# Kernel tuning notes

Hardware: AMD Instinct MI355X
Metric: run time of the kernel (lower is better)

Reference implementation:

```python
import jax, jax.numpy as jnp
import numpy as np

FS = 44100
LS = 1323000  # 30 s at 44.1 kHz (Ls/fs = 30 exactly)
FMIN, FMAX, BNDS = 32.7, 20000.0, 96
MIN_WIN = 4


def _design():
    """Reimplementation of LogScale + nsgfwin(sliced=False) + calcwinrange +
    the matrixform nsgtf loop parameters, producing a dense gather-index
    matrix idx [nbins, Mmax] and window matrix gw [nbins, Mmax]."""
    odiv = (np.log2(FMAX) - np.log2(FMIN)) / (BNDS - 1)
    pow2n = 2.0 ** odiv
    f = FMIN * pow2n ** np.arange(BNDS)
    lbas = BNDS
    frqs = np.concatenate(([0.0], f, [FS / 2.0]))
    fbas = np.concatenate((frqs, FS - frqs[-2:0:-1]))  # mirror negative freqs
    fbas *= float(LS) / FS
    # bandwidths M (window lengths)
    M = np.zeros(len(fbas), dtype=np.int64)
    M[0] = np.round(2 * fbas[1])
    for k in range(1, 2 * lbas + 1):
        M[k] = np.round(fbas[k + 1] - fbas[k - 1])
    M[-1] = np.round(LS - fbas[-2])
    M = np.maximum(M, MIN_WIN)
    # Hann windows (zero-frequency centered, hannwin)
    g = [0.5 * (np.cos(np.arange(m) * (2.0 * np.pi / m)) + 1.0) for m in M]
    # center positions rfbas (calcwinrange -> timepos == rfbas, nn == Ls)
    fb = fbas.copy()
    fb[lbas] = (fbas[lbas - 1] + fbas[lbas + 1]) / 2
    fb[lbas + 2] = LS - fb[lbas]
    rfbas = np.round(fb).astype(np.int64)
    nbins = len(g) // 2 + 1        # real=True, reducedform=0
    Mmax = int(M[:nbins].max())    # matrixform: all bins padded to Mmax
    idx = np.zeros((nbins, Mmax), dtype=np.int32)
    gw = np.zeros((nbins, Mmax), dtype=np.float32)
    for j in range(nbins):
        gj = g[j]
        Lg = len(gj)
        win = (np.arange(-(Lg // 2), Lg - (Lg // 2)) + rfbas[j]) % LS
        gs = np.fft.fftshift(gj)  # g is real -> conj is a no-op
        h1, h2 = (Lg + 1) // 2, Lg // 2
        # nsgtf placement: temp[:h1] = t[h2:], temp[-h2:] = t[:h2]
        idx[j, :h1] = win[h2:]
        gw[j, :h1] = gs[h2:]
        if h2 > 0:
            idx[j, Mmax - h2:] = win[:h2]
            gw[j, Mmax - h2:] = gs[:h2]
    return idx, gw


def setup_inputs() -> dict:
    key = jax.random.key(0)
    idx, gw = _design()
    s = jax.random.normal(key, (2, LS), dtype=jnp.float32)  # [channels, Ls]
    return {"s": s, "idx": jnp.asarray(idx), "gw": jnp.asarray(gw)}


def reference(s, idx, gw):
    # NSGT forward (nsgtf, matrixform, real): FFT the signal, gather each
    # frequency bin's circular window range, multiply by the fftshifted
    # window, zero-pad into a length-Mmax buffer, and IFFT per bin.
    ft = jnp.fft.fft(s.astype(jnp.complex64))          # [B, Ls]
    t = ft[:, idx] * gw                                # [B, nbins, Mmax]
    c = jnp.fft.ifft(t, axis=-1)                       # complex coefficients
    # pack complex output as trailing (real, imag) float32 channel
    return jnp.stack((c.real, c.imag), axis=-1)        # [B, nbins, Mmax, 2]
```

## Files before the change

### kernel.cpp

```cpp
#include <hip/hip_runtime.h>

#define LS 1323000
#define NB 98
#define MM 123000
#define N2 3000
#define BATCH 2
#define NROWS_T (NB*BATCH)
#define TWO_PI 6.28318530717958647692f

#define KBN 188
#define QN  96
#define SROW (KBN*QN*16)
#define QP  104

typedef __attribute__((ext_vector_type(8))) short short8;
typedef __attribute__((ext_vector_type(4))) float f32x4;

__device__ __forceinline__ float2 cmul(float2 a, float2 b){
  return make_float2(a.x*b.x - a.y*b.y, a.x*b.y + a.y*b.x);
}
__device__ __forceinline__ unsigned short f2bf(float f){
  unsigned int u = __float_as_uint(f);
  unsigned int r = (u + 0x7FFFu + ((u >> 16) & 1u)) >> 16;
  return (unsigned short)r;
}

template<int R,int S>
__device__ __forceinline__ void butterfly(float2* v){
  if constexpr (R==2){
    float2 a=v[0], b=v[1];
    v[0]=make_float2(a.x+b.x, a.y+b.y);
    v[1]=make_float2(a.x-b.x, a.y-b.y);
  } else if constexpr (R==4){
    float2 t0=make_float2(v[0].x+v[2].x, v[0].y+v[2].y);
    float2 t1=make_float2(v[0].x-v[2].x, v[0].y-v[2].y);
    float2 t2=make_float2(v[1].x+v[3].x, v[1].y+v[3].y);
    float2 t3=make_float2(v[1].x-v[3].x, v[1].y-v[3].y);
    v[0]=make_float2(t0.x+t2.x, t0.y+t2.y);
    v[2]=make_float2(t0.x-t2.x, t0.y-t2.y);
    v[1]=make_float2(t1.x - (float)S*t3.y, t1.y + (float)S*t3.x);
    v[3]=make_float2(t1.x + (float)S*t3.y, t1.y - (float)S*t3.x);
  } else if constexpr (R==8){
    float2 e[4]={v[0],v[2],v[4],v[6]};
    float2 o[4]={v[1],v[3],v[5],v[7]};
    butterfly<4,S>(e);
    butterfly<4,S>(o);
    const float h = 0.70710678118654752440f;
    float2 w1=make_float2(h, (float)S*h);
    float2 w2=make_float2(0.f, (float)S);
    float2 w3=make_float2(-h, (float)S*h);
    float2 o1=cmul(o[1],w1), o2=cmul(o[2],w2), o3=cmul(o[3],w3);
    v[0]=make_float2(e[0].x+o[0].x, e[0].y+o[0].y);
    v[4]=make_float2(e[0].x-o[0].x, e[0].y-o[0].y);
    v[1]=make_float2(e[1].x+o1.x, e[1].y+o1.y);
    v[5]=make_float2(e[1].x-o1.x, e[1].y-o1.y);
    v[2]=make_float2(e[2].x+o2.x, e[2].y+o2.y);
    v[6]=make_float2(e[2].x-o2.x, e[2].y-o2.y);
    v[3]=make_float2(e[3].x+o3.x, e[3].y+o3.y);
    v[7]=make_float2(e[3].x-o3.x, e[7-4].y-o3.y);
    v[7]=make_float2(e[3].x-o3.x, e[3].y-o3.y);
  } else {
    float2 x[R];
    #pragma unroll
    for(int k=0;k<R;k++){
      float2 acc=v[0];
      #pragma unroll
      for(int n=1;n<R;n++){
        const int p=(k*n)%R;
        float ang = (float)S * (TWO_PI/(float)R) * (float)p;
        float sn,cs; __sincosf(ang,&sn,&cs);
        acc.x += v[n].x*cs - v[n].y*sn;
        acc.y += v[n].x*sn + v[n].y*cs;
      }
      x[k]=acc;
    }
    #pragma unroll
    for(int k=0;k<R;k++) v[k]=x[k];
  }
}

template<int R,int S>
__global__ void __launch_bounds__(256)
fft_pass(const float2* __restrict__ in, float2* __restrict__ out,
         int N, int Ns, int nrows){
  const int T = N / R;
  long long gid = (long long)blockIdx.x*blockDim.x + threadIdx.x;
  if (gid >= (long long)T*nrows) return;
  int row = (int)(gid / T);
  int j   = (int)(gid - (long long)row*T);
  const float2* x = in  + (size_t)row*N;
  float2*       y = out + (size_t)row*N;
  int t = j % Ns;
  float u = (float)t / (float)(Ns*R);
  float ang = (float)S * TWO_PI * u;
  float sn,cs; __sincosf(ang,&sn,&cs);
  float2 w1=make_float2(cs,sn);
  float2 wr=make_float2(1.f,0.f);
  float2 v[R];
  #pragma unroll
  for(int r=0;r<R;r++){
    float2 a = x[j + r*T];
    v[r] = cmul(a, wr);
    wr = cmul(wr, w1);
  }
  butterfly<R,S>(v);
  int d = (j/Ns)*(Ns*R) + t;
  #pragma unroll
  for(int r=0;r<R;r++) y[d + r*Ns] = v[r];
}

__global__ void __launch_bounds__(256)
fft_r2c8(const float* __restrict__ s, float2* __restrict__ y){
  const int T = LS/8;
  long long gid = (long long)blockIdx.x*blockDim.x + threadIdx.x;
  if (gid >= (long long)T*BATCH) return;
  int row = (int)(gid / T);
  int j   = (int)(gid - (long long)row*T);
  const float* x = s + (size_t)row*LS;
  float2*      yr = y + (size_t)row*LS;
  float2 v[8];
  #pragma unroll
  for(int r=0;r<8;r++) v[r] = make_float2(x[j + r*T], 0.f);
  butterfly<8,-1>(v);
  int d = 8*j;
  #pragma unroll
  for(int r=0;r<8;r++) yr[d + r] = v[r];
}

__global__ void span_init(int* __restrict__ spanA, int* __restrict__ spanB){
  int j = blockIdx.x*blockDim.x + threadIdx.x;
  if (j < NB){ spanA[j] = 0; spanB[j] = MM; }
}

#define SPAN_SLICE 4096
__global__ void __launch_bounds__(256)
rowspan_par(const float* __restrict__ gw, int* __restrict__ spanA,
            int* __restrict__ spanB){
  const int j  = blockIdx.x;
  const int lo = blockIdx.y * SPAN_SLICE;
  const int end = min(lo + SPAN_SLICE, MM);
  const float* g = gw + (size_t)j*MM;
  const int tid = threadIdx.x;
  int mA = -1, mB = MM;
  for (int m = lo + tid*4; m < end; m += 256*4){
    float4 v = *(const float4*)(g + m);
    #pragma unroll
    for (int t = 0; t < 4; t++){
      float f = ((const float*)&v)[t];
      int m2 = m + t;
      if (f != 0.f){
        if (m2 < 61500){ if (m2 > mA) mA = m2; }
        else           { if (m2 < mB) mB = m2; }
      }
    }
  }
  __shared__ int sA[256], sB[256];
  sA[tid]=mA; sB[tid]=mB; __syncthreads();
  for (int s=128; s>0; s>>=1){
    if (tid<s){ sA[tid]=max(sA[tid],sA[tid+s]); sB[tid]=min(sB[tid],sB[tid+s]); }
    __syncthreads();
  }
  if (tid==0){
    if (sA[0] >= 0) atomicMax(&spanA[j], sA[0]+1);
    if (sB[0] < MM) atomicMin(&spanB[j], sB[0]);
  }
}

__global__ void __launch_bounds__(256)
a_prep(unsigned short* __restrict__ A96){
  int i = blockIdx.x*blockDim.x + threadIdx.x;
  if (i >= 96*QP) return;
  int R = i / QP, q = i - R*QP;
  float val = 0.f;
  if (R < 82 && q < 82){
    int k2 = R >> 1, c = R & 1, n2 = q >> 1, cp = q & 1;
    int p = (k2*n2) % 41;
    float ang = (float)p * (TWO_PI/41.f);
    float sn, cs; __sincosf(ang, &sn, &cs);
    val = c ? (cp ? cs : sn) : (cp ? -sn : cs);
  }
  A96[i] = f2bf(val);
}

#define PTILE 1681
__global__ void __launch_bounds__(256)
pack_gather(const float2* __restrict__ ft, const int* __restrict__ idx,
            const float* __restrict__ gw, const int* __restrict__ spanA,
            const int* __restrict__ spanB, float2* __restrict__ T, int row0){
  const int row  = row0 + blockIdx.y;
  const int jrow = row % NB;
  const int b    = row / NB;
  const int spA = spanA[jrow], spB = spanB[jrow];
  const int base = blockIdx.x * PTILE;
  const int end  = min(base + PTILE, MM);
  if (!(base < spA || end > spB)) return;
  __shared__ float2 tile[PTILE];
  const int cnt = end - base;
  const int*   idxr = idx + (size_t)jrow*MM;
  const float* gwr  = gw  + (size_t)jrow*MM;
  const float2* ftb = ft  + (size_t)b*LS;
  for (int l = threadIdx.x; l < cnt; l += 256){
    int n = base + l;
    float g = gwr[n] * (1.0f/(float)MM);
    float2 f = ftb[idxr[n]];
    tile[l] = make_float2(f.x*g, f.y*g);
  }
  __syncthreads();
  float2* Trow = T + (size_t)blockIdx.y*MM;
  const int bm = base % 41;
  for (int l2 = threadIdx.x; l2 < PTILE; l2 += 256){
    int n2 = l2 / 41, w = l2 - 41*n2;
    int l0 = n2 - bm; if (l0 < 0) l0 += 41;
    int l = l0 + 41*w;
    if (l < cnt){
      int n = base + l;
      if (n < spA || n >= spB){
        int ig = n / 41;
        Trow[(size_t)n2*N2 + ig] = tile[l];
      }
    }
  }
}

template<int R, int Ns>
__device__ __forceinline__ void lds_stage(const float2* src, float2* dst, int tid){
  const int T = N2 / R;
  for (int j = tid; j < T; j += 256){
    int t = j % Ns;
    float2 w1;
    if constexpr (Ns == 1) w1 = make_float2(1.f, 0.f);
    else {
      float ang = TWO_PI * (float)t / (float)(Ns*R);
      float sn, cs; __sincosf(ang, &sn, &cs);
      w1 = make_float2(cs, sn);
    }
    float2 wr = make_float2(1.f, 0.f);
    float2 v[R];
    #pragma unroll
    for (int r = 0; r < R; r++){ v[r] = cmul(src[j + r*T], wr); wr = cmul(wr, w1); }
    butterfly<R,1>(v);
    int d = (j/Ns)*(Ns*R) + t;
    #pragma unroll
    for (int r = 0; r < R; r++) dst[d + r*Ns] = v[r];
  }
}

__global__ void __launch_bounds__(256)
inv_s1(const float2* __restrict__ T, const int* __restrict__ spanA,
       const int* __restrict__ spanB,
       unsigned short* __restrict__ Bb, int row0){
  __shared__ float2 u0[N2];
  __shared__ float2 u1[N2];
  const int n2  = blockIdx.x;
  const int row = row0 + blockIdx.y;
  const int jrow = row % NB;
  const int tid = threadIdx.x;
  const int spA = spanA[jrow], spB = spanB[jrow];
  const int n1A = (spA - n2 + 40) / 41;
  const int n1B = (spB - n2 + 40) / 41;
  const float2* Trow = T + (size_t)blockIdx.y*MM + (size_t)n2*N2;
  for (int i = tid; i < N2; i += 256){
    float2 val = make_float2(0.f, 0.f);
    if (i < n1A || i >= n1B) val = Trow[i];
    u0[i] = val;
  }
  __syncthreads();
  lds_stage<5,1>(u0, u1, tid);   __syncthreads();
  lds_stage<5,5>(u1, u0, tid);   __syncthreads();
  lds_stage<5,25>(u0, u1, tid);  __syncthreads();
  lds_stage<3,125>(u1, u0, tid); __syncthreads();
  lds_stage<8,375>(u0, u1, tid); __syncthreads();
  unsigned short* Brow = Bb + (size_t)blockIdx.y*SROW;
  const int qr = 2*n2, qi = 2*n2+1;
  for (int k1 = tid; k1 < N2; k1 += 256){
    float ang = (float)(n2*k1) * (TWO_PI/(float)MM);
    float sn, cs; __sincosf(ang, &sn, &cs);
    float2 v = cmul(u1[k1], make_float2(cs, sn));
    int kb = k1 >> 4, kl = k1 & 15;
    size_t base = (size_t)kb*(QN*16) + kl;
    Brow[base + qr*16] = f2bf(v.x);
    Brow[base + qi*16] = f2bf(v.y);
  }
}

__global__ void __launch_bounds__(256)
inv_s2_mfma(const unsigned short* __restrict__ A96,
            const unsigned short* __restrict__ Bb,
            float2* __restrict__ out){
  __shared__ unsigned short Als[96*QP];
  __shared__ unsigned short Bls[64*QP];
  const int tid = threadIdx.x;

  {
    const uint4* src = (const uint4*)A96;
    uint4* dst = (uint4*)Als;
    for (int f = tid; f < (96*QP*2)/16; f += 256) dst[f] = src[f];
  }
  {
    const unsigned short* Bt = Bb + (size_t)blockIdx.y*SROW
                                  + (size_t)blockIdx.x*4*(QN*16);
    for (int f = tid; f < 768; f += 256){
      uint4 d = *(const uint4*)(Bt + (size_t)f*8);
      int q   = (f >> 1) % QN;
      int kb  = f / (QN*2);
      int kl0 = (f & 1) * 8;
      if (q >= 82) d = make_uint4(0u,0u,0u,0u);
      const unsigned short* e = (const unsigned short*)&d;
      int rbase = kb*16 + kl0;
      #pragma unroll
      for (int j = 0; j < 8; j++)
        Bls[(rbase + j)*QP + q] = e[j];
    }
  }
  __syncthreads();

  const int w = tid >> 6, l = tid & 63;
  const int g = l >> 4, c = l & 15;

  f32x4 acc[6];
  #pragma unroll
  for (int m = 0; m < 6; m++) acc[m] = (f32x4){0.f,0.f,0.f,0.f};

  short8 b0 = *(const short8*)&Bls[(16*w + c)*QP +  0 + 8*g];
  short8 b1 = *(const short8*)&Bls[(16*w + c)*QP + 32 + 8*g];
  short8 b2 = *(const short8*)&Bls[(16*w + c)*QP + 64 + 8*g];
  #pragma unroll
  for (int m = 0; m < 6; m++){
    short8 a0 = *(const short8*)&Als[(16*m + c)*QP +  0 + 8*g];
    short8 a1 = *(const short8*)&Als[(16*m + c)*QP + 32 + 8*g];
    short8 a2 = *(const short8*)&Als[(16*m + c)*QP + 64 + 8*g];
    acc[m] = __builtin_amdgcn_mfma_f32_16x16x32_bf16(a0, b0, acc[m], 0, 0, 0);
    acc[m] = __builtin_amdgcn_mfma_f32_16x16x32_bf16(a1, b1, acc[m], 0, 0, 0);
    acc[m] = __builtin_amdgcn_mfma_f32_16x16x32_bf16(a2, b2, acc[m], 0, 0, 0);
  }

  float2* orow = out + (size_t)blockIdx.y*MM;
  int k1 = blockIdx.x*64 + 16*w + c;
  if (k1 < N2){
    #pragma unroll
    for (int m = 0; m < 6; m++){
      int R0 = 16*m + 4*g;
      int k2a = R0 >> 1;
      int k2b = k2a + 1;
      if (k2a < 41) orow[(size_t)k2a*N2 + k1] = make_float2(acc[m][0], acc[m][1]);
      if (k2b < 41) orow[(size_t)k2b*N2 + k1] = make_float2(acc[m][2], acc[m][3]);
    }
  }
}

extern "C" void kernel_launch(void* const* d_in, const int* in_sizes, int n_in,
                              void* d_out, int out_size, void* d_ws, size_t ws_size,
                              hipStream_t stream){
  const float* s   = (const float*)d_in[0];
  const int*   idx = (const int*)d_in[1];
  const float* gw  = (const float*)d_in[2];
  float2* out = (float2*)d_out;
  char* ws = (char*)d_ws;

  const size_t FWD_BYTES = 21168128;
  float2* bufA = (float2*)ws;
  float2* bufB = (float2*)(ws + FWD_BYTES);
  int* spanA = (int*)(ws + 2*FWD_BYTES);
  int* spanB = (int*)(ws + 2*FWD_BYTES + 512);
  unsigned short* A96 = (unsigned short*)(ws + 2*FWD_BYTES + 1024);
  const size_t A_BYTES = 20480;
  unsigned short* Bbase = (unsigned short*)(ws + 2*FWD_BYTES + 1024 + A_BYTES);

  a_prep<<<(96*QP + 255)/256, 256, 0, stream>>>(A96);
  span_init<<<1, 128, 0, stream>>>(spanA, spanB);
  {
    dim3 g(NB, (MM + SPAN_SLICE - 1)/SPAN_SLICE);
    rowspan_par<<<g, 256, 0, stream>>>(gw, spanA, spanB);
  }

  {
    long long tot = (long long)(LS/8)*BATCH;
    int blks = (int)((tot + 255)/256);
    fft_r2c8<<<blks,256,0,stream>>>(s, bufA);
  }
  float2* cur = bufA; float2* nxt = bufB;
  int Ns = 8;
  #define FWD(R) do{                                                         \
    long long tot = (long long)(LS/(R))*BATCH;                               \
    int blks = (int)((tot + 255)/256);                                       \
    fft_pass<R,-1><<<blks,256,0,stream>>>(cur, nxt, LS, Ns, BATCH);          \
    Ns *= (R);                                                               \
    { float2* tmp=cur; cur=nxt; nxt=tmp; }                                   \
  }while(0)
  FWD(7); FWD(7); FWD(5); FWD(5); FWD(5); FWD(3); FWD(3); FWD(3);
  #undef FWD

  const size_t row_bytes = (size_t)SROW * 2;
  size_t used = 2*FWD_BYTES + 1024 + A_BYTES;
  size_t avail = (ws_size > used) ? (ws_size - used) : 0;
  int max_chunk = (int)(avail / row_bytes);
  if (max_chunk > NROWS_T) max_chunk = NROWS_T;
  if (max_chunk < 1) max_chunk = 1;

  const int ptiles = (MM + PTILE - 1)/PTILE;
  for (int c0 = 0; c0 < NROWS_T; c0 += max_chunk){
    int cr = NROWS_T - c0; if (cr > max_chunk) cr = max_chunk;
    float2* Tchunk = out + (size_t)c0*MM;
    dim3 g0(ptiles, cr);
    pack_gather<<<g0,256,0,stream>>>(cur, idx, gw, spanA, spanB, Tchunk, c0);
    dim3 g1(41, cr);
    inv_s1<<<g1,256,0,stream>>>(Tchunk, spanA, spanB, Bbase, c0);
    dim3 g2(47, cr);
    inv_s2_mfma<<<g2,256,0,stream>>>(A96, Bbase, Tchunk);
  }
}
```

Measured before the change: 542.7 us.

## Pack both real channels into one complex FFT and precompute inverse twiddle tables

```diff
diff --git a/kernel.cpp b/kernel.cpp
--- a/kernel.cpp
+++ b/kernel.cpp
@@ -13,6 +13,12 @@
 #define SROW (KBN*QN*16)
 #define QP  104
 
+#define TBL2_OFF 0
+#define TBL3_OFF 20
+#define TBL4_OFF 120
+#define TBL5_OFF 370
+#define TBL_N    2995
+
 typedef __attribute__((ext_vector_type(8))) short short8;
 typedef __attribute__((ext_vector_type(4))) float f32x4;
 
@@ -27,11 +33,7 @@
 
 template<int R,int S>
 __device__ __forceinline__ void butterfly(float2* v){
-  if constexpr (R==2){
-    float2 a=v[0], b=v[1];
-    v[0]=make_float2(a.x+b.x, a.y+b.y);
-    v[1]=make_float2(a.x-b.x, a.y-b.y);
-  } else if constexpr (R==4){
+  if constexpr (R==4){
     float2 t0=make_float2(v[0].x+v[2].x, v[0].y+v[2].y);
     float2 t1=make_float2(v[0].x-v[2].x, v[0].y-v[2].y);
     float2 t2=make_float2(v[1].x+v[3].x, v[1].y+v[3].y);
@@ -57,7 +59,6 @@
     v[2]=make_float2(e[2].x+o2.x, e[2].y+o2.y);
     v[6]=make_float2(e[2].x-o2.x, e[2].y-o2.y);
     v[3]=make_float2(e[3].x+o3.x, e[3].y+o3.y);
-    v[7]=make_float2(e[3].x-o3.x, e[7-4].y-o3.y);
     v[7]=make_float2(e[3].x-o3.x, e[3].y-o3.y);
   } else {
     float2 x[R];
@@ -82,14 +83,10 @@
 template<int R,int S>
 __global__ void __launch_bounds__(256)
 fft_pass(const float2* __restrict__ in, float2* __restrict__ out,
-         int N, int Ns, int nrows){
+         int N, int Ns){
   const int T = N / R;
-  long long gid = (long long)blockIdx.x*blockDim.x + threadIdx.x;
-  if (gid >= (long long)T*nrows) return;
-  int row = (int)(gid / T);
-  int j   = (int)(gid - (long long)row*T);
-  const float2* x = in  + (size_t)row*N;
-  float2*       y = out + (size_t)row*N;
+  int j = blockIdx.x*blockDim.x + threadIdx.x;
+  if (j >= T) return;
   int t = j % Ns;
   float u = (float)t / (float)(Ns*R);
   float ang = (float)S * TWO_PI * u;
@@ -99,32 +96,30 @@
   float2 v[R];
   #pragma unroll
   for(int r=0;r<R;r++){
-    float2 a = x[j + r*T];
+    float2 a = in[j + r*T];
     v[r] = cmul(a, wr);
     wr = cmul(wr, w1);
   }
   butterfly<R,S>(v);
   int d = (j/Ns)*(Ns*R) + t;
   #pragma unroll
-  for(int r=0;r<R;r++) y[d + r*Ns] = v[r];
-}
-
-__global__ void __launch_bounds__(256)
-fft_r2c8(const float* __restrict__ s, float2* __restrict__ y){
+  for(int r=0;r<R;r++) out[d + r*Ns] = v[r];
+}
+
+__global__ void __launch_bounds__(256)
+fft_c2c8(const float* __restrict__ s, float2* __restrict__ y){
   const int T = LS/8;
-  long long gid = (long long)blockIdx.x*blockDim.x + threadIdx.x;
-  if (gid >= (long long)T*BATCH) return;
-  int row = (int)(gid / T);
-  int j   = (int)(gid - (long long)row*T);
-  const float* x = s + (size_t)row*LS;
-  float2*      yr = y + (size_t)row*LS;
+  int j = blockIdx.x*blockDim.x + threadIdx.x;
+  if (j >= T) return;
+  const float* x0 = s;
+  const float* x1 = s + LS;
   float2 v[8];
   #pragma unroll
-  for(int r=0;r<8;r++) v[r] = make_float2(x[j + r*T], 0.f);
+  for(int r=0;r<8;r++) v[r] = make_float2(x0[j + r*T], x1[j + r*T]);
   butterfly<8,-1>(v);
   int d = 8*j;
   #pragma unroll
-  for(int r=0;r<8;r++) yr[d + r] = v[r];
+  for(int r=0;r<8;r++) y[d + r] = v[r];
 }
 
 __global__ void span_init(int* __restrict__ spanA, int* __restrict__ spanB){
@@ -176,10 +171,24 @@
     int k2 = R >> 1, c = R & 1, n2 = q >> 1, cp = q & 1;
     int p = (k2*n2) % 41;
     float ang = (float)p * (TWO_PI/41.f);
-    float sn, cs; __sincosf(ang, &sn, &cs);
+    float sn, cs; sincosf(ang, &sn, &cs);
     val = c ? (cp ? cs : sn) : (cp ? -sn : cs);
   }
   A96[i] = f2bf(val);
+}
+
+__global__ void __launch_bounds__(256)
+twid_prep(float2* __restrict__ tbl){
+  int i = blockIdx.x*blockDim.x + threadIdx.x;
+  if (i >= TBL_N) return;
+  int t, r, den;
+  if (i < TBL3_OFF)      { int l=i;          t=l/4; r=l%4+1; den=25;   }
+  else if (i < TBL4_OFF) { int l=i-TBL3_OFF; t=l/4; r=l%4+1; den=125;  }
+  else if (i < TBL5_OFF) { int l=i-TBL4_OFF; t=l/2; r=l%2+1; den=375;  }
+  else                   { int l=i-TBL5_OFF; t=l/7; r=l%7+1; den=3000; }
+  float ang = TWO_PI * (float)(t*r) / (float)den;
+  float sn, cs; sincosf(ang, &sn, &cs);
+  tbl[i] = make_float2(cs, sn);
 }
 
 #define PTILE 1681
@@ -198,11 +207,15 @@
   const int cnt = end - base;
   const int*   idxr = idx + (size_t)jrow*MM;
   const float* gwr  = gw  + (size_t)jrow*MM;
-  const float2* ftb = ft  + (size_t)b*LS;
   for (int l = threadIdx.x; l < cnt; l += 256){
     int n = base + l;
     float g = gwr[n] * (1.0f/(float)MM);
-    float2 f = ftb[idxr[n]];
+    int id = idxr[n];
+    float2 F1 = ft[id];
+    float2 F2 = ft[id ? (LS - id) : 0];
+    float2 f;
+    if (b == 0) f = make_float2(0.5f*(F1.x + F2.x), 0.5f*(F1.y - F2.y));
+    else        f = make_float2(0.5f*(F1.y + F2.y), 0.5f*(F2.x - F1.x));
     tile[l] = make_float2(f.x*g, f.y*g);
   }
   __syncthreads();
@@ -222,22 +235,31 @@
   }
 }
 
+template<int R>
+__device__ __forceinline__ void lds_stage1(const float2* src, float2* dst, int tid){
+  const int T = N2 / R;
+  for (int j = tid; j < T; j += 256){
+    float2 v[R];
+    #pragma unroll
+    for (int r = 0; r < R; r++) v[r] = src[j + r*T];
+    butterfly<R,1>(v);
+    int d = j*R;
+    #pragma unroll
+    for (int r = 0; r < R; r++) dst[d + r] = v[r];
+  }
+}
+
 template<int R, int Ns>
-__device__ __forceinline__ void lds_stage(const float2* src, float2* dst, int tid){
+__device__ __forceinline__ void lds_stage_t(const float2* src, float2* dst,
+                                            int tid, const float2* tw){
   const int T = N2 / R;
   for (int j = tid; j < T; j += 256){
     int t = j % Ns;
-    float2 w1;
-    if constexpr (Ns == 1) w1 = make_float2(1.f, 0.f);
-    else {
-      float ang = TWO_PI * (float)t / (float)(Ns*R);
-      float sn, cs; __sincosf(ang, &sn, &cs);
-      w1 = make_float2(cs, sn);
-    }
-    float2 wr = make_float2(1.f, 0.f);
+    const float2* w = tw + t*(R-1);
     float2 v[R];
-    #pragma unroll
-    for (int r = 0; r < R; r++){ v[r] = cmul(src[j + r*T], wr); wr = cmul(wr, w1); }
+    v[0] = src[j];
+    #pragma unroll
+    for (int r = 1; r < R; r++) v[r] = cmul(src[j + r*T], w[r-1]);
     butterfly<R,1>(v);
     int d = (j/Ns)*(Ns*R) + t;
     #pragma unroll
@@ -247,13 +269,13 @@
 
 __global__ void __launch_bounds__(256)
 inv_s1(const float2* __restrict__ T, const int* __restrict__ spanA,
-       const int* __restrict__ spanB,
+       const int* __restrict__ spanB, const float2* __restrict__ tbl,
        unsigned short* __restrict__ Bb, int row0){
   __shared__ float2 u0[N2];
   __shared__ float2 u1[N2];
+  __shared__ float2 tlds[TBL5_OFF];
   const int n2  = blockIdx.x;
-  const int row = row0 + blockIdx.y;
-  const int jrow = row % NB;
+  const int jrow = (row0 + blockIdx.y) % NB;
   const int tid = threadIdx.x;
   const int spA = spanA[jrow], spB = spanB[jrow];
   const int n1A = (spA - n2 + 40) / 41;
@@ -264,22 +286,39 @@
     if (i < n1A || i >= n1B) val = Trow[i];
     u0[i] = val;
   }
+  for (int i = tid; i < TBL5_OFF; i += 256) tlds[i] = tbl[i];
   __syncthreads();
-  lds_stage<5,1>(u0, u1, tid);   __syncthreads();
-  lds_stage<5,5>(u1, u0, tid);   __syncthreads();
-  lds_stage<5,25>(u0, u1, tid);  __syncthreads();
-  lds_stage<3,125>(u1, u0, tid); __syncthreads();
-  lds_stage<8,375>(u0, u1, tid); __syncthreads();
+  lds_stage1<5>(u0, u1, tid);                          __syncthreads();
+  lds_stage_t<5,5>  (u1, u0, tid, tlds + TBL2_OFF);    __syncthreads();
+  lds_stage_t<5,25> (u0, u1, tid, tlds + TBL3_OFF);    __syncthreads();
+  lds_stage_t<3,125>(u1, u0, tid, tlds + TBL4_OFF);    __syncthreads();
+
   unsigned short* Brow = Bb + (size_t)blockIdx.y*SROW;
+  const float2* tbl5 = tbl + TBL5_OFF;
   const int qr = 2*n2, qi = 2*n2+1;
-  for (int k1 = tid; k1 < N2; k1 += 256){
-    float ang = (float)(n2*k1) * (TWO_PI/(float)MM);
-    float sn, cs; __sincosf(ang, &sn, &cs);
-    float2 v = cmul(u1[k1], make_float2(cs, sn));
-    int kb = k1 >> 4, kl = k1 & 15;
-    size_t base = (size_t)kb*(QN*16) + kl;
-    Brow[base + qr*16] = f2bf(v.x);
-    Brow[base + qi*16] = f2bf(v.y);
+  float sn, cs;
+  __sincosf((float)(n2*375) * (TWO_PI/(float)MM), &sn, &cs);
+  const float2 wstep = make_float2(cs, sn);
+  for (int j = tid; j < 375; j += 256){
+    const float2* w = tbl5 + j*7;
+    float2 v[8];
+    v[0] = u0[j];
+    #pragma unroll
+    for (int r = 1; r < 8; r++) v[r] = cmul(u0[j + r*375], w[r-1]);
+    butterfly<8,1>(v);
+    float ang = (float)(n2*j) * (TWO_PI/(float)MM);
+    __sincosf(ang, &sn, &cs);
+    float2 wf = make_float2(cs, sn);
+    #pragma unroll
+    for (int r = 0; r < 8; r++){
+      float2 o = cmul(v[r], wf);
+      int k1 = j + 375*r;
+      int kb = k1 >> 4, kl = k1 & 15;
+      size_t base = (size_t)kb*(QN*16) + kl;
+      Brow[base + qr*16] = f2bf(o.x);
+      Brow[base + qi*16] = f2bf(o.y);
+      wf = cmul(wf, wstep);
+    }
   }
 }
 
@@ -357,16 +396,19 @@
   float2* out = (float2*)d_out;
   char* ws = (char*)d_ws;
 
-  const size_t FWD_BYTES = 21168128;
+  const size_t FWD_BYTES = 10584064;
   float2* bufA = (float2*)ws;
   float2* bufB = (float2*)(ws + FWD_BYTES);
   int* spanA = (int*)(ws + 2*FWD_BYTES);
   int* spanB = (int*)(ws + 2*FWD_BYTES + 512);
   unsigned short* A96 = (unsigned short*)(ws + 2*FWD_BYTES + 1024);
   const size_t A_BYTES = 20480;
-  unsigned short* Bbase = (unsigned short*)(ws + 2*FWD_BYTES + 1024 + A_BYTES);
+  float2* tbl = (float2*)(ws + 2*FWD_BYTES + 1024 + A_BYTES);
+  const size_t TBL_BYTES = 24576;
+  unsigned short* Bbase = (unsigned short*)(ws + 2*FWD_BYTES + 1024 + A_BYTES + TBL_BYTES);
 
   a_prep<<<(96*QP + 255)/256, 256, 0, stream>>>(A96);
+  twid_prep<<<(TBL_N + 255)/256, 256, 0, stream>>>(tbl);
   span_init<<<1, 128, 0, stream>>>(spanA, spanB);
   {
     dim3 g(NB, (MM + SPAN_SLICE - 1)/SPAN_SLICE);
@@ -374,16 +416,14 @@
   }
 
   {
-    long long tot = (long long)(LS/8)*BATCH;
-    int blks = (int)((tot + 255)/256);
-    fft_r2c8<<<blks,256,0,stream>>>(s, bufA);
+    int blks = (LS/8 + 255)/256;
+    fft_c2c8<<<blks,256,0,stream>>>(s, bufA);
   }
   float2* cur = bufA; float2* nxt = bufB;
   int Ns = 8;
   #define FWD(R) do{                                                         \
-    long long tot = (long long)(LS/(R))*BATCH;                               \
-    int blks = (int)((tot + 255)/256);                                       \
-    fft_pass<R,-1><<<blks,256,0,stream>>>(cur, nxt, LS, Ns, BATCH);          \
+    int blks = (LS/(R) + 255)/256;                                           \
+    fft_pass<R,-1><<<blks,256,0,stream>>>(cur, nxt, LS, Ns);                 \
     Ns *= (R);                                                               \
     { float2* tmp=cur; cur=nxt; nxt=tmp; }                                   \
   }while(0)
@@ -391,7 +431,7 @@
   #undef FWD
 
   const size_t row_bytes = (size_t)SROW * 2;
-  size_t used = 2*FWD_BYTES + 1024 + A_BYTES;
+  size_t used = 2*FWD_BYTES + 1024 + A_BYTES + TBL_BYTES;
   size_t avail = (ws_size > used) ? (ws_size - used) : 0;
   int max_chunk = (int)(avail / row_bytes);
   if (max_chunk > NROWS_T) max_chunk = NROWS_T;
@@ -404,7 +444,7 @@
     dim3 g0(ptiles, cr);
     pack_gather<<<g0,256,0,stream>>>(cur, idx, gw, spanA, spanB, Tchunk, c0);
     dim3 g1(41, cr);
-    inv_s1<<<g1,256,0,stream>>>(Tchunk, spanA, spanB, Bbase, c0);
+    inv_s1<<<g1,256,0,stream>>>(Tchunk, spanA, spanB, tbl, Bbase, c0);
     dim3 g2(47, cr);
     inv_s2_mfma<<<g2,256,0,stream>>>(A96, Bbase, Tchunk);
   }
```

Result: faster. 515.0 us (-5.1%).
